# Kernel tuning notes

Measured on AMD Instinct MI355X. Metric: run time of the kernel, lower is better.

## Reference

```python
import jax, jax.numpy as jnp
import numpy as np

NUM_HEADS = 8
NEG_INF = -2**32 + 1  # matches the TF code's masking constant


def setup_inputs() -> dict:
    key = jax.random.key(0)
    ks = jax.random.split(key, 12)
    B, L, D_IN, D_MODEL = 2, 2048, 256, 256
    s = 1.0 / np.sqrt(D_IN)
    return {
        "queries": jax.random.normal(ks[0], (B, L, D_IN), jnp.float32),
        "keys": jax.random.normal(ks[1], (B, L, D_IN), jnp.float32),
        "values": jax.random.normal(ks[2], (B, L, D_IN), jnp.float32),
        "key_mask": jax.random.randint(ks[3], (B, L, 1), 0, 2, jnp.int32),
        "Wq": jax.random.normal(ks[4], (D_IN, D_MODEL), jnp.float32) * s,
        "bq": jnp.zeros((D_MODEL,), jnp.float32),
        "Wk": jax.random.normal(ks[5], (D_IN, D_MODEL), jnp.float32) * s,
        "bk": jnp.zeros((D_MODEL,), jnp.float32),
        "Wv": jax.random.normal(ks[6], (D_IN, D_MODEL), jnp.float32) * s,
        "bv": jnp.zeros((D_MODEL,), jnp.float32),
        "Wo": jax.random.normal(ks[7], (D_MODEL, D_IN), jnp.float32) * s,
        "bo": jnp.zeros((D_IN,), jnp.float32),
    }


def reference(queries, keys, values, key_mask, Wq, bq, Wk, bk, Wv, bv, Wo, bo):
    B, Lq, _ = queries.shape
    Lk = keys.shape[1]
    h = NUM_HEADS
    d_model = Wq.shape[1]
    depth = d_model // h

    Q = queries @ Wq + bq  # [B, Lq, d_model]
    K = keys @ Wk + bk     # [B, Lk, d_model]
    V = values @ Wv + bv   # [B, Lk, d_model]

    # split heads: contiguous chunks of size depth along feature dim
    Qh = Q.reshape(B, Lq, h, depth)
    Kh = K.reshape(B, Lk, h, depth)
    Vh = V.reshape(B, Lk, h, depth)

    scores = jnp.einsum("bqhd,bkhd->bhqk", Qh, Kh) / jnp.sqrt(
        jnp.asarray(depth, jnp.float32)
    )  # [B, h, Lq, Lk]

    # key_mask: [B, Lk, 1] -> broadcast over heads and query positions
    mask = (key_mask[:, None, :, 0] != 0)[:, :, None, :]  # [B, 1, 1, Lk]
    scores = jnp.where(mask, scores, jnp.asarray(NEG_INF, scores.dtype))

    attn = jax.nn.softmax(scores, axis=-1)  # dropout is identity at inference
    out = jnp.einsum("bhqk,bkhd->bqhd", attn, Vh).reshape(B, Lq, d_model)
    return out @ Wo + bo  # [B, Lq, input_dim]
```

## Files before the change

kernel.cpp:

```cpp
#include <hip/hip_runtime.h>

#define Bn 2
#define Ln 2048
#define DIN 256
#define Hn 8
#define DEPTH 32
#define SCALE 0.17677669529663687f
#define NEGC (-4294967296.0f)

typedef _Float16 f16;
typedef _Float16 h8 __attribute__((ext_vector_type(8)));
typedef _Float16 h4 __attribute__((ext_vector_type(4)));
typedef float f4 __attribute__((ext_vector_type(4)));

#define WLS 264


__global__ __launch_bounds__(256) void proj_gemm(
    const float* __restrict__ Xq, const float* __restrict__ Xk, const float* __restrict__ Xv,
    const float* __restrict__ Wq, const float* __restrict__ Wk, const float* __restrict__ Wv,
    const float* __restrict__ bq, const float* __restrict__ bk, const float* __restrict__ bv,
    f16* __restrict__ Qb, f16* __restrict__ Kb, f16* __restrict__ Vt)
{
    __shared__ f16 Wl[64 * WLS];
    const int p = blockIdx.z;
    const float* X = p == 0 ? Xq : p == 1 ? Xk : Xv;
    const float* W = p == 0 ? Wq : p == 1 ? Wk : Wv;
    const float* bias = p == 0 ? bq : p == 1 ? bk : bv;

    const int t = threadIdx.x, w = t >> 6, lane = t & 63;
    const int l15 = lane & 15, quad = lane >> 4;
    const int n0 = blockIdx.y * 64;

    {
        const int nl = t & 63, kb = t >> 6;
        for (int kk = 0; kk < 64; ++kk) {
            const int k = kk * 4 + kb;
            Wl[nl * WLS + k] = (f16)W[(size_t)k * DIN + n0 + nl];
        }
    }
    __syncthreads();

    const int m0w = blockIdx.x * 128 + w * 32;
    const float* A0 = X + (size_t)(m0w + l15) * DIN;
    const float* A1 = X + (size_t)(m0w + 16 + l15) * DIN;

    f4 acc[2][4];
    #pragma unroll
    for (int mi = 0; mi < 2; ++mi)
        #pragma unroll
        for (int tt = 0; tt < 4; ++tt) acc[mi][tt] = (f4){0.f, 0.f, 0.f, 0.f};

    for (int k0 = 0; k0 < DIN; k0 += 32) {
        float4 xa0 = *(const float4*)(A0 + k0 + quad * 8);
        float4 xb0 = *(const float4*)(A0 + k0 + quad * 8 + 4);
        float4 xa1 = *(const float4*)(A1 + k0 + quad * 8);
        float4 xb1 = *(const float4*)(A1 + k0 + quad * 8 + 4);
        h8 af0 = { (f16)xa0.x, (f16)xa0.y, (f16)xa0.z, (f16)xa0.w,
                   (f16)xb0.x, (f16)xb0.y, (f16)xb0.z, (f16)xb0.w };
        h8 af1 = { (f16)xa1.x, (f16)xa1.y, (f16)xa1.z, (f16)xa1.w,
                   (f16)xb1.x, (f16)xb1.y, (f16)xb1.z, (f16)xb1.w };
        #pragma unroll
        for (int tt = 0; tt < 4; ++tt) {
            h8 bf = *(const h8*)(Wl + (tt * 16 + l15) * WLS + k0 + quad * 8);
            acc[0][tt] = __builtin_amdgcn_mfma_f32_16x16x32_f16(af0, bf, acc[0][tt], 0, 0, 0);
            acc[1][tt] = __builtin_amdgcn_mfma_f32_16x16x32_f16(af1, bf, acc[1][tt], 0, 0, 0);
        }
    }
    #pragma unroll
    for (int mi = 0; mi < 2; ++mi)
        #pragma unroll
        for (int tt = 0; tt < 4; ++tt) {
            const int c = n0 + tt * 16 + l15;
            const float bb = bias[c];
            const int h = c >> 5, dd = c & 31;
            #pragma unroll
            for (int r = 0; r < 4; ++r) {
                const int row = m0w + mi * 16 + quad * 4 + r;
                const int b = row >> 11, l = row & (Ln - 1);
                const float v = acc[mi][tt][r] + bb;
                if (p == 0)
                    Qb[(((size_t)(b * Hn + h)) * Ln + l) * DEPTH + dd] = (f16)(v * SCALE);
                else if (p == 1)
                    Kb[(((size_t)(b * Hn + h)) * Ln + l) * DEPTH + dd] = (f16)v;
                else
                    Vt[(((size_t)(b * Hn + h)) * DEPTH + dd) * Ln + l] = (f16)v;
            }
        }
}

__global__ __launch_bounds__(256) void flash_mfma(
    const f16* __restrict__ Qb, const f16* __restrict__ Kb,
    const f16* __restrict__ Vt, const int* __restrict__ mask,
    f16* __restrict__ Ob)
{
    __shared__ float Os[4][32][34];
    __shared__ float lS[4][32];
    const int t = threadIdx.x, w = t >> 6, lane = t & 63;
    const int l15 = lane & 15, quad = lane >> 4;
    const int hb = blockIdx.x;
    const int q0 = blockIdx.y * 32;
    const int b = hb >> 3;
    const f16* Qh = Qb + (size_t)hb * Ln * DEPTH;
    const f16* Kh = Kb + (size_t)hb * Ln * DEPTH;
    const f16* Vh = Vt + (size_t)hb * DEPTH * Ln;
    const int* mrow = mask + b * Ln;
    const int k_base = w * (Ln / 4);

    const h8 qf0 = *(const h8*)(Qh + (size_t)(q0 + l15) * DEPTH + quad * 8);
    const h8 qf1 = *(const h8*)(Qh + (size_t)(q0 + 16 + l15) * DEPTH + quad * 8);

    f4 o[2][2];
    #pragma unroll
    for (int i = 0; i < 2; ++i)
        #pragma unroll
        for (int j = 0; j < 2; ++j) o[i][j] = (f4){0.f, 0.f, 0.f, 0.f};
    float l_run[2] = {0.f, 0.f};

    for (int kt = 0; kt < Ln / 4 / 64; ++kt) {
        const int k0 = k_base + kt * 64;
        f4 s[4][2];
        h4 va[4][2];
        #pragma unroll
        for (int tt = 0; tt < 4; ++tt) {
            h8 kf = *(const h8*)(Kh + (size_t)(k0 + tt * 16 + l15) * DEPTH + quad * 8);
            const int4 mk = *(const int4*)(mrow + k0 + tt * 16 + quad * 4);
            f4 bias4 = { mk.x ? 0.f : NEGC, mk.y ? 0.f : NEGC,
                         mk.z ? 0.f : NEGC, mk.w ? 0.f : NEGC };
            s[tt][0] = __builtin_amdgcn_mfma_f32_16x16x32_f16(kf, qf0, bias4, 0, 0, 0);
            s[tt][1] = __builtin_amdgcn_mfma_f32_16x16x32_f16(kf, qf1, bias4, 0, 0, 0);
            va[tt][0] = *(const h4*)(Vh + (size_t)l15 * Ln        + k0 + tt * 16 + quad * 4);
            va[tt][1] = *(const h4*)(Vh + (size_t)(16 + l15) * Ln + k0 + tt * 16 + quad * 4);
        }
        #pragma unroll
        for (int tt = 0; tt < 4; ++tt)
            #pragma unroll
            for (int qg = 0; qg < 2; ++qg) {
                h4 pf;
                #pragma unroll
                for (int r = 0; r < 4; ++r) {
                    const float pv = __expf(s[tt][qg][r]);
                    l_run[qg] += pv;
                    pf[r] = (f16)pv;
                }
                o[0][qg] = __builtin_amdgcn_mfma_f32_16x16x16f16(va[tt][0], pf, o[0][qg], 0, 0, 0);
                o[1][qg] = __builtin_amdgcn_mfma_f32_16x16x16f16(va[tt][1], pf, o[1][qg], 0, 0, 0);
            }
    }
    #pragma unroll
    for (int qg = 0; qg < 2; ++qg) {
        l_run[qg] += __shfl_xor(l_run[qg], 16, 64);
        l_run[qg] += __shfl_xor(l_run[qg], 32, 64);
        if (quad == 0) lS[w][qg * 16 + l15] = l_run[qg];
        #pragma unroll
        for (int dg = 0; dg < 2; ++dg)
            #pragma unroll
            for (int r = 0; r < 4; ++r)
                Os[w][dg * 16 + quad * 4 + r][qg * 16 + l15] = o[dg][qg][r];
    }
    __syncthreads();

    {
        const int cq = t & 31, d0 = t >> 5;
        const float ls = lS[0][cq] + lS[1][cq] + lS[2][cq] + lS[3][cq];
        const float inv = 1.0f / ls;
        f16* Oq = Ob + ((size_t)hb * Ln + q0 + cq) * DEPTH;
        #pragma unroll
        for (int i = 0; i < 4; ++i) {
            const int dd = d0 + 8 * i;
            const float ov = Os[0][dd][cq] + Os[1][dd][cq] +
                             Os[2][dd][cq] + Os[3][dd][cq];
            Oq[dd] = (f16)(ov * inv);
        }
    }
}

__global__ __launch_bounds__(256) void out_gemm(
    const f16* __restrict__ Ob, const float* __restrict__ Wo,
    const float* __restrict__ bo, float* __restrict__ out)
{
    __shared__ f16 Wl[64 * WLS];
    const int t = threadIdx.x, w = t >> 6, lane = t & 63;
    const int l15 = lane & 15, quad = lane >> 4;
    const int m0 = blockIdx.x * 64 + w * 16;
    const int n0 = blockIdx.y * 64;

    {
        const int nl = t & 63, kb = t >> 6;
        for (int kk = 0; kk < 64; ++kk) {
            const int k = kk * 4 + kb;
            Wl[nl * WLS + k] = (f16)Wo[(size_t)k * DIN + n0 + nl];
        }
    }
    __syncthreads();

    const int rA = m0 + l15, bA = rA >> 11, qA = rA & (Ln - 1);

    f4 acc[4] = {{0.f,0.f,0.f,0.f},{0.f,0.f,0.f,0.f},{0.f,0.f,0.f,0.f},{0.f,0.f,0.f,0.f}};
    for (int k0 = 0; k0 < DIN; k0 += 32) {
        const int h = k0 >> 5;
        h8 af = *(const h8*)(Ob + (((size_t)(bA * Hn + h)) * Ln + qA) * DEPTH + quad * 8);
        #pragma unroll
        for (int tt = 0; tt < 4; ++tt) {
            h8 bf = *(const h8*)(Wl + (tt * 16 + l15) * WLS + k0 + quad * 8);
            acc[tt] = __builtin_amdgcn_mfma_f32_16x16x32_f16(af, bf, acc[tt], 0, 0, 0);
        }
    }
    #pragma unroll
    for (int tt = 0; tt < 4; ++tt) {
        const int c = n0 + tt * 16 + l15;
        const float bb = bo[c];
        #pragma unroll
        for (int r = 0; r < 4; ++r)
            out[(size_t)(m0 + quad * 4 + r) * DIN + c] = acc[tt][r] + bb;
    }
}

#define QT 128
#define KT 32
#define TS 34
#define SST (KT + 1)

__global__ __launch_bounds__(512) void fb_fused_attn(
    const float* __restrict__ Xq, const float* __restrict__ Xk,
    const float* __restrict__ Xv, const int* __restrict__ mask,
    const float* __restrict__ Wq, const float* __restrict__ bq,
    const float* __restrict__ Wk, const float* __restrict__ bk,
    const float* __restrict__ Wv, const float* __restrict__ bv,
    float* __restrict__ out)
{
    __shared__ float Qs[QT * TS];
    __shared__ float Ks[KT * TS];
    __shared__ float Vs[KT * TS];
    __shared__ float Ss[QT * SST];
    __shared__ float mrow[QT], lrow[QT], arow[QT];
    __shared__ int mk[KT];

    const int t = threadIdx.x;
    const int d = t & 31;
    const int rg = t >> 5;
    const int q0 = blockIdx.x * QT;
    const int h = blockIdx.y;
    const int b = blockIdx.z;
    const int hc = h * DEPTH + d;

    {
        const float bqv = bq[hc];
        for (int i = 0; i < 8; ++i) {
            const int r = rg + 16 * i;
            const float* x = Xq + ((size_t)(b * Ln + q0 + r)) * DIN;
            float acc = bqv;
            #pragma unroll 8
            for (int k = 0; k < DIN; ++k) acc = fmaf(x[k], Wq[k * DIN + hc], acc);
            Qs[r * TS + d] = acc * SCALE;
        }
    }
    if (t < QT) { mrow[t] = -INFINITY; lrow[t] = 0.f; }
    float o_acc[8];
    #pragma unroll
    for (int i = 0; i < 8; ++i) o_acc[i] = 0.f;

    const float bkv = bk[hc], bvv = bv[hc];

    for (int kt = 0; kt < Ln / KT; ++kt) {
        const int k0 = kt * KT;
        #pragma unroll
        for (int i = 0; i < 2; ++i) {
            const int r = rg + 16 * i;
            const float* xk = Xk + ((size_t)(b * Ln + k0 + r)) * DIN;
            const float* xv = Xv + ((size_t)(b * Ln + k0 + r)) * DIN;
            float aK = bkv, aV = bvv;
            #pragma unroll 4
            for (int k = 0; k < DIN; ++k) {
                aK = fmaf(xk[k], Wk[k * DIN + hc], aK);
                aV = fmaf(xv[k], Wv[k * DIN + hc], aV);
            }
            Ks[r * TS + d] = aK;
            Vs[r * TS + d] = aV;
        }
        if (t < KT) mk[t] = mask[b * Ln + k0 + t];
        __syncthreads();

        for (int idx = t; idx < QT * KT; idx += 512) {
            const int r = idx >> 5, k = idx & (KT - 1);
            const float2* qv = (const float2*)(Qs + r * TS);
            const float2* kv = (const float2*)(Ks + k * TS);
            float s = 0.f;
            #pragma unroll
            for (int j = 0; j < 16; ++j) {
                float2 a = qv[j], c = kv[j];
                s += a.x * c.x + a.y * c.y;
            }
            Ss[r * SST + k] = mk[k] ? s : NEGC;
        }
        __syncthreads();

        if (t < QT) {
            float tm = -INFINITY;
            #pragma unroll 8
            for (int k = 0; k < KT; ++k) tm = fmaxf(tm, Ss[t * SST + k]);
            const float nm = fmaxf(mrow[t], tm);
            arow[t] = __expf(mrow[t] - nm);
            mrow[t] = nm;
        }
        __syncthreads();

        for (int idx = t; idx < QT * KT; idx += 512) {
            const int r = idx >> 5, k = idx & (KT - 1);
            Ss[r * SST + k] = __expf(Ss[r * SST + k] - mrow[r]);
        }
        __syncthreads();

        if (t < QT) {
            float rs = 0.f;
            #pragma unroll 8
            for (int k = 0; k < KT; ++k) rs += Ss[t * SST + k];
            lrow[t] = arow[t] * lrow[t] + rs;
        }
        #pragma unroll
        for (int i = 0; i < 8; ++i) {
            const int r = rg + 16 * i;
            const float a = arow[r];
            float acc = o_acc[i] * a;
            const float* pr = Ss + r * SST;
            const float* vc = Vs + d;
            #pragma unroll 8
            for (int k = 0; k < KT; ++k) acc = fmaf(pr[k], vc[k * TS], acc);
            o_acc[i] = acc;
        }
        __syncthreads();
    }
    #pragma unroll
    for (int i = 0; i < 8; ++i) {
        const int r = rg + 16 * i;
        out[((size_t)(b * Ln + q0 + r)) * DIN + hc] = o_acc[i] / lrow[r];
    }
}

__global__ __launch_bounds__(256) void fb_out_proj(
    const float* __restrict__ Wo, const float* __restrict__ bo,
    float* __restrict__ out)
{
    __shared__ float xr[4][DIN];
    const int col = threadIdx.x;
    const int r0 = blockIdx.x * 4;
    #pragma unroll
    for (int rr = 0; rr < 4; ++rr)
        xr[rr][col] = out[(size_t)(r0 + rr) * DIN + col];
    __syncthreads();
    const float bb = bo[col];
    float a0 = bb, a1 = bb, a2 = bb, a3 = bb;
    #pragma unroll 4
    for (int k = 0; k < DIN; ++k) {
        const float w = Wo[k * DIN + col];
        a0 = fmaf(xr[0][k], w, a0);
        a1 = fmaf(xr[1][k], w, a1);
        a2 = fmaf(xr[2][k], w, a2);
        a3 = fmaf(xr[3][k], w, a3);
    }
    float* o = out + (size_t)r0 * DIN + col;
    o[0] = a0; o[DIN] = a1; o[2 * DIN] = a2; o[3 * DIN] = a3;
}

extern "C" void kernel_launch(void* const* d_in, const int* in_sizes, int n_in,
                              void* d_out, int out_size, void* d_ws, size_t ws_size,
                              hipStream_t stream) {
    const float* Xq = (const float*)d_in[0];
    const float* Xk = (const float*)d_in[1];
    const float* Xv = (const float*)d_in[2];
    const int* mask = (const int*)d_in[3];
    const float* Wq = (const float*)d_in[4];
    const float* bq = (const float*)d_in[5];
    const float* Wk = (const float*)d_in[6];
    const float* bk = (const float*)d_in[7];
    const float* Wv = (const float*)d_in[8];
    const float* bv = (const float*)d_in[9];
    const float* Wo = (const float*)d_in[10];
    const float* bo = (const float*)d_in[11];
    float* out = (float*)d_out;

    const size_t HB_E = (size_t)Bn * Hn * Ln * DEPTH;
    const size_t need = 3 * HB_E * sizeof(f16);

    if (ws_size >= need) {
        f16* Qb = (f16*)d_ws;
        f16* Kb = Qb + HB_E;
        f16* Vt = Kb + HB_E;
        proj_gemm<<<dim3(Bn * Ln / 128, DIN / 64, 3), 256, 0, stream>>>(
            Xq, Xk, Xv, Wq, Wk, Wv, bq, bk, bv, Qb, Kb, Vt);
        flash_mfma<<<dim3(Bn * Hn, Ln / 32), 256, 0, stream>>>(Qb, Kb, Vt, mask, Qb);
        out_gemm<<<dim3(Bn * Ln / 64, DIN / 64), 256, 0, stream>>>(Qb, Wo, bo, out);
    } else {
        fb_fused_attn<<<dim3(Ln / QT, Hn, Bn), 512, 0, stream>>>(
            Xq, Xk, Xv, mask, Wq, bq, Wk, bk, Wv, bv, out);
        fb_out_proj<<<Bn * Ln / 4, 256, 0, stream>>>(Wo, bo, out);
    }
}
```

Before: 144.9 us.

## Double query tile per flash block to reuse K/V loads across more queries

Each flash_mfma block now handles 64 queries instead of 32, keeping four Q fragments per wave so every K, V and mask load feeds twice as many MFMAs. The grid halves to Ln/64 blocks per head, the score/V staging arrays are replaced by per-tile temporaries, and the final output is written as packed 8-half vectors. The aim is less global K/V traffic per query. In exchange it raises register and LDS use and leaves fewer blocks to fill the GPU.

```diff
diff --git a/kernel.cpp b/kernel.cpp
--- a/kernel.cpp
+++ b/kernel.cpp
@@ -94,12 +94,12 @@
     const f16* __restrict__ Vt, const int* __restrict__ mask,
     f16* __restrict__ Ob)
 {
-    __shared__ float Os[4][32][34];
-    __shared__ float lS[4][32];
+    __shared__ float Os[4][32][68];
+    __shared__ float lS[4][64];
     const int t = threadIdx.x, w = t >> 6, lane = t & 63;
     const int l15 = lane & 15, quad = lane >> 4;
     const int hb = blockIdx.x;
-    const int q0 = blockIdx.y * 32;
+    const int q0 = blockIdx.y * 64;
     const int b = hb >> 3;
     const f16* Qh = Qb + (size_t)hb * Ln * DEPTH;
     const f16* Kh = Kb + (size_t)hb * Ln * DEPTH;
@@ -107,48 +107,48 @@
     const int* mrow = mask + b * Ln;
     const int k_base = w * (Ln / 4);
 
-    const h8 qf0 = *(const h8*)(Qh + (size_t)(q0 + l15) * DEPTH + quad * 8);
-    const h8 qf1 = *(const h8*)(Qh + (size_t)(q0 + 16 + l15) * DEPTH + quad * 8);
-
-    f4 o[2][2];
+    h8 qf[4];
+    #pragma unroll
+    for (int qg = 0; qg < 4; ++qg)
+        qf[qg] = *(const h8*)(Qh + (size_t)(q0 + qg * 16 + l15) * DEPTH + quad * 8);
+
+    f4 o[2][4];
     #pragma unroll
     for (int i = 0; i < 2; ++i)
         #pragma unroll
-        for (int j = 0; j < 2; ++j) o[i][j] = (f4){0.f, 0.f, 0.f, 0.f};
-    float l_run[2] = {0.f, 0.f};
+        for (int j = 0; j < 4; ++j) o[i][j] = (f4){0.f, 0.f, 0.f, 0.f};
+    float l_run[4] = {0.f, 0.f, 0.f, 0.f};
 
     for (int kt = 0; kt < Ln / 4 / 64; ++kt) {
         const int k0 = k_base + kt * 64;
-        f4 s[4][2];
-        h4 va[4][2];
         #pragma unroll
         for (int tt = 0; tt < 4; ++tt) {
             h8 kf = *(const h8*)(Kh + (size_t)(k0 + tt * 16 + l15) * DEPTH + quad * 8);
             const int4 mk = *(const int4*)(mrow + k0 + tt * 16 + quad * 4);
             f4 bias4 = { mk.x ? 0.f : NEGC, mk.y ? 0.f : NEGC,
                          mk.z ? 0.f : NEGC, mk.w ? 0.f : NEGC };
-            s[tt][0] = __builtin_amdgcn_mfma_f32_16x16x32_f16(kf, qf0, bias4, 0, 0, 0);
-            s[tt][1] = __builtin_amdgcn_mfma_f32_16x16x32_f16(kf, qf1, bias4, 0, 0, 0);
-            va[tt][0] = *(const h4*)(Vh + (size_t)l15 * Ln        + k0 + tt * 16 + quad * 4);
-            va[tt][1] = *(const h4*)(Vh + (size_t)(16 + l15) * Ln + k0 + tt * 16 + quad * 4);
-        }
-        #pragma unroll
-        for (int tt = 0; tt < 4; ++tt)
-            #pragma unroll
-            for (int qg = 0; qg < 2; ++qg) {
+            h4 va0 = *(const h4*)(Vh + (size_t)l15 * Ln        + k0 + tt * 16 + quad * 4);
+            h4 va1 = *(const h4*)(Vh + (size_t)(16 + l15) * Ln + k0 + tt * 16 + quad * 4);
+            f4 s[4];
+            #pragma unroll
+            for (int qg = 0; qg < 4; ++qg)
+                s[qg] = __builtin_amdgcn_mfma_f32_16x16x32_f16(kf, qf[qg], bias4, 0, 0, 0);
+            #pragma unroll
+            for (int qg = 0; qg < 4; ++qg) {
                 h4 pf;
                 #pragma unroll
                 for (int r = 0; r < 4; ++r) {
-                    const float pv = __expf(s[tt][qg][r]);
+                    const float pv = __expf(s[qg][r]);
                     l_run[qg] += pv;
                     pf[r] = (f16)pv;
                 }
-                o[0][qg] = __builtin_amdgcn_mfma_f32_16x16x16f16(va[tt][0], pf, o[0][qg], 0, 0, 0);
-                o[1][qg] = __builtin_amdgcn_mfma_f32_16x16x16f16(va[tt][1], pf, o[1][qg], 0, 0, 0);
+                o[0][qg] = __builtin_amdgcn_mfma_f32_16x16x16f16(va0, pf, o[0][qg], 0, 0, 0);
+                o[1][qg] = __builtin_amdgcn_mfma_f32_16x16x16f16(va1, pf, o[1][qg], 0, 0, 0);
             }
-    }
-    #pragma unroll
-    for (int qg = 0; qg < 2; ++qg) {
+        }
+    }
+    #pragma unroll
+    for (int qg = 0; qg < 4; ++qg) {
         l_run[qg] += __shfl_xor(l_run[qg], 16, 64);
         l_run[qg] += __shfl_xor(l_run[qg], 32, 64);
         if (quad == 0) lS[w][qg * 16 + l15] = l_run[qg];
@@ -161,17 +161,18 @@
     __syncthreads();
 
     {
-        const int cq = t & 31, d0 = t >> 5;
+        const int cq = t & 63, dv = t >> 6;
         const float ls = lS[0][cq] + lS[1][cq] + lS[2][cq] + lS[3][cq];
         const float inv = 1.0f / ls;
-        f16* Oq = Ob + ((size_t)hb * Ln + q0 + cq) * DEPTH;
-        #pragma unroll
-        for (int i = 0; i < 4; ++i) {
-            const int dd = d0 + 8 * i;
+        h8 pack;
+        #pragma unroll
+        for (int i = 0; i < 8; ++i) {
+            const int dd = dv * 8 + i;
             const float ov = Os[0][dd][cq] + Os[1][dd][cq] +
                              Os[2][dd][cq] + Os[3][dd][cq];
-            Oq[dd] = (f16)(ov * inv);
-        }
+            pack[i] = (f16)(ov * inv);
+        }
+        *(h8*)(Ob + ((size_t)hb * Ln + q0 + cq) * DEPTH + dv * 8) = pack;
     }
 }
 
@@ -388,7 +389,7 @@
         f16* Vt = Kb + HB_E;
         proj_gemm<<<dim3(Bn * Ln / 128, DIN / 64, 3), 256, 0, stream>>>(
             Xq, Xk, Xv, Wq, Wk, Wv, bq, bk, bv, Qb, Kb, Vt);
-        flash_mfma<<<dim3(Bn * Hn, Ln / 32), 256, 0, stream>>>(Qb, Kb, Vt, mask, Qb);
+        flash_mfma<<<dim3(Bn * Hn, Ln / 64), 256, 0, stream>>>(Qb, Kb, Vt, mask, Qb);
         out_gemm<<<dim3(Bn * Ln / 64, DIN / 64), 256, 0, stream>>>(Qb, Wo, bo, out);
     } else {
         fb_fused_attn<<<dim3(Ln / QT, Hn, Bn), 512, 0, stream>>>(
```

Measured after the change: 126.4 us. 12.8% less time.
